# Kernel optimization log

Hardware: AMD Instinct MI355X
Metric: run time of the kernel (lower is better)

## Reference

```python
import jax, jax.numpy as jnp
import numpy as np

NUM_IN_CAPS = 1152   # 32 * 6 * 6
NUM_OUT_CAPS = 10
IN_DIM = 8
OUT_DIM = 16
ROUTING_ITERS = 3
EPS = 1e-8


def squash(s, axis=-1):
    # squash(s) = ||s||^2/(1+||s||^2) * s/||s||
    sq = jnp.sum(s * s, axis=axis, keepdims=True)
    norm = jnp.sqrt(sq + EPS)
    return (sq / (1.0 + sq)) * (s / norm)


def setup_inputs() -> dict:
    key = jax.random.key(0)
    ks = jax.random.split(key, 6)
    B = 512
    inp = jax.random.uniform(ks[0], (B, 1, 28, 28), dtype=jnp.float32)
    # conv params (He-ish scale)
    conv1_w = jax.random.normal(ks[1], (256, 1, 9, 9), dtype=jnp.float32) * 0.05
    conv1_b = jnp.zeros((256,), dtype=jnp.float32)
    conv2_w = jax.random.normal(ks[2], (256, 256, 9, 9), dtype=jnp.float32) * 0.01
    conv2_b = jnp.zeros((256,), dtype=jnp.float32)
    # capsule transform weights: [in_caps, out_caps, in_dim, out_dim]
    cap_W = jax.random.normal(ks[3], (NUM_IN_CAPS, NUM_OUT_CAPS, IN_DIM, OUT_DIM), dtype=jnp.float32) * 0.05
    return {"input": inp, "conv1_w": conv1_w, "conv1_b": conv1_b,
            "conv2_w": conv2_w, "conv2_b": conv2_b, "cap_W": cap_W}


def _conv(x, w, b, stride):
    y = jax.lax.conv_general_dilated(
        x, w, window_strides=(stride, stride), padding='VALID',
        dimension_numbers=('NCHW', 'OIHW', 'NCHW'))
    return y + b[None, :, None, None]


def capsnet_forward(input, conv1_w, conv1_b, conv2_w, conv2_b, cap_W):
    B = input.shape[0]
    h = jax.nn.relu(_conv(input, conv1_w, conv1_b, 1))   # [B,256,20,20]
    h = _conv(h, conv2_w, conv2_b, 2)                    # [B,256,6,6]
    # torch.transpose(output, 1, -1): [B,C,H,W] -> [B,W,H,C], then view(B,1152,8)
    u = jnp.transpose(h, (0, 3, 2, 1)).reshape(B, NUM_IN_CAPS, IN_DIM)
    # predicted output vectors u_hat: [B, i, j, q]
    u_hat = jnp.einsum('bip,ijpq->bijq', u, cap_W)
    # dynamic routing
    b_ij = jnp.zeros((B, NUM_IN_CAPS, NUM_OUT_CAPS), dtype=u_hat.dtype)
    v = None
    for _ in range(ROUTING_ITERS):
        c = jax.nn.softmax(b_ij, axis=2)                 # coupling over output caps
        s = jnp.einsum('bij,bijq->bjq', c, u_hat)        # [B, j, q]
        v = squash(s)                                    # [B, j, q]
        b_ij = b_ij + jnp.einsum('bijq,bjq->bij', u_hat, v)
    return v  # [B, 10, 16]


def reference(input, conv1_w, conv1_b, conv2_w, conv2_b, cap_W):
    return capsnet_forward(input, conv1_w, conv1_b, conv2_w, conv2_b, cap_W)
```

## Files before the change

### kernel.cpp

```cpp
#include <hip/hip_runtime.h>
#include <hip/hip_bf16.h>

typedef __attribute__((ext_vector_type(8))) short bf16x8;
typedef __attribute__((ext_vector_type(4))) float f32x4;

static __device__ __forceinline__ unsigned short f2bf(float x) {
    __hip_bfloat16 h = __float2bfloat16(x);
    return *(unsigned short*)&h;
}
static __device__ __forceinline__ float bflo(unsigned int w) { return __uint_as_float(w << 16); }
static __device__ __forceinline__ float bfhi(unsigned int w) { return __uint_as_float(w & 0xffff0000u); }
static __device__ __forceinline__ float bf1(unsigned short u) { return __uint_as_float(((unsigned int)u) << 16); }

typedef __attribute__((address_space(1))) const void gvoid;
typedef __attribute__((address_space(3))) void lvoid;
static __device__ __forceinline__ void gl_lds16(const void* g, void* l) {
    __builtin_amdgcn_global_load_lds((gvoid*)g, (lvoid*)l, 16, 0, 0);
}

#define PART_FLOATS 4718592

__global__ __launch_bounds__(320) void conv1_k(const float* __restrict__ in,
                                               const float* __restrict__ w,
                                               const float* __restrict__ bias,
                                               unsigned short* __restrict__ h1n) {
    int blk = blockIdx.x;
    int b = blk >> 4;
    int c0 = (blk & 15) * 16;
    __shared__ float img[784];
    __shared__ float wl[16 * 81];
    __shared__ float bl[16];
    __shared__ unsigned short tr[20 * 328];
    int tid = threadIdx.x;
    for (int t = tid; t < 784; t += 320) img[t] = in[b * 784 + t];
    for (int t = tid; t < 1296; t += 320) wl[t] = w[c0 * 81 + t];
    if (tid < 16) bl[tid] = bias[c0 + tid];
    __syncthreads();

    int co = tid / 20, oy = tid % 20;
    float wr[81];
#pragma unroll
    for (int k = 0; k < 81; k++) wr[k] = wl[co * 81 + k];
    float acc[20];
    float bv = bl[co];
#pragma unroll
    for (int ox = 0; ox < 20; ox++) acc[ox] = bv;

#pragma unroll
    for (int ky = 0; ky < 9; ky++) {
        const float* rp = &img[(oy + ky) * 28];
        float r[28];
#pragma unroll
        for (int v = 0; v < 7; v++) {
            float4 t4 = ((const float4*)rp)[v];
            r[v * 4 + 0] = t4.x; r[v * 4 + 1] = t4.y;
            r[v * 4 + 2] = t4.z; r[v * 4 + 3] = t4.w;
        }
#pragma unroll
        for (int kx = 0; kx < 9; kx++) {
            float wv = wr[ky * 9 + kx];
#pragma unroll
            for (int ox = 0; ox < 20; ox++) acc[ox] += r[ox + kx] * wv;
        }
    }
#pragma unroll
    for (int ox = 0; ox < 20; ox++)
        tr[oy * 328 + ox * 16 + co] = f2bf(fmaxf(acc[ox], 0.f));
    __syncthreads();
    for (int g = tid; g < 800; g += 320) {
        int p = g >> 1, half = g & 1;
        uint4 v = *(uint4*)&tr[(p / 20) * 328 + (p % 20) * 16 + half * 8];
        *(uint4*)&h1n[(b * 400 + p) * 256 + c0 + half * 8] = v;
    }
}

__global__ __launch_bounds__(256) void wt2_k(const float* __restrict__ w2,
                                             unsigned short* __restrict__ Wt2) {
    int cout = blockIdx.x;
    int ci = threadIdx.x;
    const float* src = w2 + (cout * 256 + ci) * 81;
#pragma unroll 1
    for (int kk = 0; kk < 81; kk++)
        Wt2[kk * 65536 + cout * 256 + ci] = f2bf(src[kk]);
#pragma unroll
    for (int kk = 81; kk < 84; kk++)
        Wt2[kk * 65536 + cout * 256 + ci] = 0;
}

__global__ __launch_bounds__(256) void wcap_k(const float* __restrict__ W,
                                              unsigned short* __restrict__ Wb) {
    int idx4 = blockIdx.x * 256 + threadIdx.x;
    float4 v = *(const float4*)&W[(size_t)idx4 * 4];
    unsigned int lo = (unsigned int)f2bf(v.x) | ((unsigned int)f2bf(v.y) << 16);
    unsigned int hi = (unsigned int)f2bf(v.z) | ((unsigned int)f2bf(v.w) << 16);
    uint2 pk; pk.x = lo; pk.y = hi;
    *(uint2*)&Wb[(size_t)idx4 * 4] = pk;
}

__global__ __launch_bounds__(256) void conv2_k(const unsigned short* __restrict__ h1n,
                                               const unsigned short* __restrict__ Wt2,
                                               const float* __restrict__ bias,
                                               float* __restrict__ u,
                                               float* __restrict__ part1,
                                               float* __restrict__ part23) {
    __shared__ unsigned short sA[2][128 * 64];
    __shared__ unsigned short sB[2][128 * 64];
    int tid = threadIdx.x;
    int m0 = blockIdx.x * 128;
    int n0 = blockIdx.y * 128;
    int slice = blockIdx.z;
    int ks = slice * 21;

    int wv = tid >> 6, lane = tid & 63;
    int wm = wv >> 1, wn = wv & 1;
    int lr = lane & 15, quad = lane >> 4;

    int lrow = lane >> 3, lslot = lane & 7;
    int kcoff = (lslot ^ lrow) * 8;
    int aG[4], bG[4];
#pragma unroll
    for (int t = 0; t < 4; t++) {
        int r = wv * 32 + t * 8 + lrow;
        int R = m0 + r;
        int b = R / 36, m = R % 36;
        int oy = m / 6, ox = m % 6;
        aG[t] = b * 102400 + oy * 10240 + ox * 512 + kcoff;
        bG[t] = (n0 + r) * 256 + kcoff;
    }

    f32x4 acc[4][4];
#pragma unroll
    for (int i = 0; i < 4; i++)
#pragma unroll
        for (int j = 0; j < 4; j++) acc[i][j] = (f32x4){0.f, 0.f, 0.f, 0.f};

    auto stage = [&](int buf, int rr) {
        int kk = ks + (rr >> 2), cr = rr & 3;
        int ky = kk / 9, kx = kk % 9;
        int aoff = ky * 5120 + kx * 256 + cr * 64;
        int boff = kk * 65536 + cr * 64;
        unsigned short* dA = &sA[buf][wv * 2048];
        unsigned short* dB = &sB[buf][wv * 2048];
#pragma unroll
        for (int t = 0; t < 4; t++)
            gl_lds16(h1n + aG[t] + aoff, dA + t * 512);
#pragma unroll
        for (int t = 0; t < 4; t++)
            gl_lds16(Wt2 + bG[t] + boff, dB + t * 512);
    };

    stage(0, 0);
    __syncthreads();

    int cur = 0;
#pragma unroll 1
    for (int rr = 0; rr < 84; rr++) {
        if (rr < 83) stage(cur ^ 1, rr + 1);
        const unsigned short* pA = &sA[cur][0];
        const unsigned short* pB = &sB[cur][0];
#pragma unroll
        for (int s = 0; s < 2; s++) {
            bf16x8 af[4], bf[4];
#pragma unroll
            for (int i = 0; i < 4; i++) {
                int arow = wm * 64 + i * 16 + lr;
                af[i] = *(bf16x8*)&pA[arow * 64 + 8 * ((s * 4 + quad) ^ (lr & 7))];
            }
#pragma unroll
            for (int j = 0; j < 4; j++) {
                int brow = wn * 64 + j * 16 + lr;
                bf[j] = *(bf16x8*)&pB[brow * 64 + 8 * ((s * 4 + quad) ^ (lr & 7))];
            }
#pragma unroll
            for (int i = 0; i < 4; i++)
#pragma unroll
                for (int j = 0; j < 4; j++)
                    acc[i][j] = __builtin_amdgcn_mfma_f32_16x16x32_bf16(
                        af[i], bf[j], acc[i][j], 0, 0, 0);
        }
        __syncthreads();
        cur ^= 1;
    }

    float* dst = (slice == 0) ? u : ((slice == 1) ? part1 : part23 + (size_t)(slice - 2) * PART_FLOATS);
#pragma unroll
    for (int j = 0; j < 4; j++) {
        int col = n0 + wn * 64 + j * 16 + lr;
        float bv = (slice == 0) ? bias[col] : 0.f;
#pragma unroll
        for (int i = 0; i < 4; i++) {
#pragma unroll
            for (int rg = 0; rg < 4; rg++) {
                int RR = m0 + wm * 64 + i * 16 + quad * 4 + rg;
                int bb = RR / 36, mm = RR % 36;
                int oyy = mm / 6, oxx = mm % 6;
                dst[bb * 9216 + oxx * 1536 + oyy * 256 + col] = acc[i][j][rg] + bv;
            }
        }
    }
}

__global__ __launch_bounds__(256) void uhat_k(const float* __restrict__ u,
                                              const float* __restrict__ p1,
                                              const float* __restrict__ p23,
                                              const unsigned short* __restrict__ Wb,
                                              unsigned short* __restrict__ uhat) {
    int i0 = blockIdx.x * 64;
    int b0 = blockIdx.y * 8;
    __shared__ float ul[8 * 576];
    __shared__ unsigned short wl[64 * 130];
    int tid = threadIdx.x;

    for (int t = tid; t < 1024; t += 256) {
        int bb = t >> 7, rq = t & 127;
        int r = rq * 4;
        size_t gidx = (size_t)(b0 + bb) * 9216 + i0 * 8 + r;
        float4 a = *(const float4*)&u[gidx];
        float4 x = *(const float4*)&p1[gidx];
        float4 y = *(const float4*)&p23[gidx];
        float4 z = *(const float4*)&p23[PART_FLOATS + gidx];
        float* d = &ul[bb * 576 + (r >> 3) * 9 + (r & 7)];
        d[0] = a.x + x.x + y.x + z.x;
        d[1] = a.y + x.y + y.y + z.y;
        d[2] = a.z + x.z + y.z + z.z;
        d[3] = a.w + x.w + y.w + z.w;
    }

    int il = tid & 63, g = tid >> 6;
    for (int j = 0; j < 10; j++) {
        __syncthreads();
        for (int t = tid; t < 4096; t += 256) {
            int li = t >> 6, cp = t & 63;
            *(unsigned int*)&wl[li * 130 + cp * 2] =
                *(const unsigned int*)&Wb[(size_t)(i0 + li) * 1280 + j * 128 + cp * 2];
        }
        __syncthreads();
#pragma unroll 1
        for (int bb = 0; bb < 8; bb++) {
            float ur[8];
#pragma unroll
            for (int p = 0; p < 8; p++) ur[p] = ul[bb * 576 + il * 9 + p];
            float a[4];
#pragma unroll
            for (int k = 0; k < 4; k++) {
                int q = g * 4 + k;
                float s = 0.f;
#pragma unroll
                for (int p = 0; p < 8; p++) s += ur[p] * bf1(wl[il * 130 + p * 16 + q]);
                a[k] = s;
            }
            unsigned int lo = (unsigned int)f2bf(a[0]) | ((unsigned int)f2bf(a[1]) << 16);
            unsigned int hi = (unsigned int)f2bf(a[2]) | ((unsigned int)f2bf(a[3]) << 16);
            uint2 pk; pk.x = lo; pk.y = hi;
            *(uint2*)&uhat[((size_t)(b0 + bb) * 10 + j) * 18432 + (size_t)(i0 + il) * 16 + g * 4] = pk;
        }
    }
}

__global__ __launch_bounds__(256) void route_k(const unsigned short* __restrict__ uhat,
                                               float* __restrict__ out) {
    int b = blockIdx.x;
    int tid = threadIdx.x;
    int w = tid >> 6, lane = tid & 63;
    int ig = lane >> 2, qh = lane & 3;
    __shared__ float b_sh[1152 * 10];
    __shared__ float s_red[4 * 160];
    __shared__ float v_sh[160];
    __shared__ float sc_sh[10];
    const unsigned short* ub = uhat + (size_t)b * 184320;

    float v_ln[10][4];

    auto finish = [&](float sp[10][4]) {
#pragma unroll
        for (int j = 0; j < 10; j++)
#pragma unroll
            for (int k = 0; k < 4; k++) {
                float t = sp[j][k];
                t += __shfl_xor(t, 4);
                t += __shfl_xor(t, 8);
                t += __shfl_xor(t, 16);
                t += __shfl_xor(t, 32);
                sp[j][k] = t;
            }
        if (ig == 0) {
#pragma unroll
            for (int j = 0; j < 10; j++) {
                f32x4 v4 = {sp[j][0], sp[j][1], sp[j][2], sp[j][3]};
                *(f32x4*)&s_red[w * 160 + j * 16 + qh * 4] = v4;
            }
        }
        __syncthreads();
        if (tid < 160) {
            float s = s_red[tid] + s_red[160 + tid] + s_red[320 + tid] + s_red[480 + tid];
            s_red[tid] = s;
        }
        __syncthreads();
        if (tid < 10) {
            float sq = 0.f;
#pragma unroll
            for (int q = 0; q < 16; q++) { float x = s_red[tid * 16 + q]; sq += x * x; }
            float norm = sqrtf(sq + 1e-8f);
            sc_sh[tid] = (sq / (1.0f + sq)) / norm;
        }
        __syncthreads();
        if (tid < 160) v_sh[tid] = s_red[tid] * sc_sh[tid >> 4];
        __syncthreads();
#pragma unroll
        for (int j = 0; j < 10; j++) {
            f32x4 v4 = *(const f32x4*)&v_sh[j * 16 + qh * 4];
            v_ln[j][0] = v4[0]; v_ln[j][1] = v4[1]; v_ln[j][2] = v4[2]; v_ln[j][3] = v4[3];
        }
        __syncthreads();
    };

    {
        float sp[10][4];
#pragma unroll
        for (int j = 0; j < 10; j++)
#pragma unroll
            for (int k = 0; k < 4; k++) sp[j][k] = 0.f;
#pragma unroll 2
        for (int r = 0; r < 18; r++) {
            int i = r * 64 + w * 16 + ig;
            const unsigned short* up = ub + (size_t)i * 16 + qh * 4;
            uint2 uh[10];
#pragma unroll
            for (int j = 0; j < 10; j++) uh[j] = *(const uint2*)(up + (size_t)j * 18432);
#pragma unroll
            for (int j = 0; j < 10; j++) {
                sp[j][0] += 0.1f * bflo(uh[j].x);
                sp[j][1] += 0.1f * bfhi(uh[j].x);
                sp[j][2] += 0.1f * bflo(uh[j].y);
                sp[j][3] += 0.1f * bfhi(uh[j].y);
            }
        }
        finish(sp);
    }

#pragma unroll 1
    for (int pass = 0; pass < 2; pass++) {
        bool first = (pass == 0);
        float sp[10][4];
#pragma unroll
        for (int j = 0; j < 10; j++)
#pragma unroll
            for (int k = 0; k < 4; k++) sp[j][k] = 0.f;
#pragma unroll 2
        for (int r = 0; r < 18; r++) {
            int i = r * 64 + w * 16 + ig;
            const unsigned short* up = ub + (size_t)i * 16 + qh * 4;
            uint2 uh[10];
#pragma unroll
            for (int j = 0; j < 10; j++) uh[j] = *(const uint2*)(up + (size_t)j * 18432);
            float d[10];
#pragma unroll
            for (int j = 0; j < 10; j++) {
                d[j] = bflo(uh[j].x) * v_ln[j][0] + bfhi(uh[j].x) * v_ln[j][1]
                     + bflo(uh[j].y) * v_ln[j][2] + bfhi(uh[j].y) * v_ln[j][3];
            }
#pragma unroll
            for (int j = 0; j < 10; j++) {
                d[j] += __shfl_xor(d[j], 1);
                d[j] += __shfl_xor(d[j], 2);
            }
            float bn[10];
            if (first) {
#pragma unroll
                for (int j = 0; j < 10; j++) bn[j] = d[j];
#pragma unroll
                for (int j = 0; j < 10; j++)
                    if (qh == (j & 3)) b_sh[i * 10 + j] = bn[j];
            } else {
#pragma unroll
                for (int j = 0; j < 10; j++) bn[j] = b_sh[i * 10 + j] + d[j];
            }
            float m = bn[0];
#pragma unroll
            for (int j = 1; j < 10; j++) m = fmaxf(m, bn[j]);
            float e[10], sum = 0.f;
#pragma unroll
            for (int j = 0; j < 10; j++) { e[j] = __expf(bn[j] - m); sum += e[j]; }
            float inv = 1.f / sum;
#pragma unroll
            for (int j = 0; j < 10; j++) {
                float c = e[j] * inv;
                sp[j][0] += c * bflo(uh[j].x);
                sp[j][1] += c * bfhi(uh[j].x);
                sp[j][2] += c * bflo(uh[j].y);
                sp[j][3] += c * bfhi(uh[j].y);
            }
        }
        finish(sp);
    }

    if (tid < 160) out[b * 160 + tid] = v_sh[tid];
}

extern "C" void kernel_launch(void* const* d_in, const int* in_sizes, int n_in,
                              void* d_out, int out_size, void* d_ws, size_t ws_size,
                              hipStream_t stream) {
    const float* input = (const float*)d_in[0];
    const float* c1w = (const float*)d_in[1];
    const float* c1b = (const float*)d_in[2];
    const float* c2w = (const float*)d_in[3];
    const float* c2b = (const float*)d_in[4];
    const float* capW = (const float*)d_in[5];
    float* out = (float*)d_out;

    const size_t U_OFF = 0;
    const size_t P1_OFF = 18874368;
    const size_t WB_OFF = 37748736;
    const size_t B_OFF = 43122688;
    const size_t WT2_BYTES = (size_t)84 * 65536 * 2;
    const size_t H1N_BYTES = 104857600;
    const size_t PART_BYTES = (size_t)PART_FLOATS * 4;
    const size_t CONV_BYTES = WT2_BYTES + H1N_BYTES + 2 * PART_BYTES;
    if (ws_size < B_OFF + CONV_BYTES) return;

    char* wsb = (char*)d_ws;
    float* u_buf = (float*)(wsb + U_OFF);
    float* part1 = (float*)(wsb + P1_OFF);
    unsigned short* Wb = (unsigned short*)(wsb + WB_OFF);
    unsigned short* Wt2 = (unsigned short*)(wsb + B_OFF);
    unsigned short* h1n = (unsigned short*)(wsb + B_OFF + WT2_BYTES);
    float* part23 = (float*)(wsb + B_OFF + WT2_BYTES + H1N_BYTES);
    unsigned short* uhatb = (unsigned short*)(wsb + B_OFF);

    wcap_k<<<1440, 256, 0, stream>>>(capW, Wb);
    wt2_k<<<256, 256, 0, stream>>>(c2w, Wt2);
    conv1_k<<<512 * 16, 320, 0, stream>>>(input, c1w, c1b, h1n);
    conv2_k<<<dim3(144, 2, 4), 256, 0, stream>>>(h1n, Wt2, c2b, u_buf, part1, part23);

    const int Cr = 256;
    for (int b0 = 0; b0 < 512; b0 += Cr) {
        uhat_k<<<dim3(18, Cr / 8), 256, 0, stream>>>(
            u_buf + (size_t)b0 * 9216, part1 + (size_t)b0 * 9216,
            part23 + (size_t)b0 * 9216, Wb, uhatb);
        route_k<<<Cr, 256, 0, stream>>>(uhatb, out + (size_t)b0 * 160);
    }
}
```

Measured before the change: 707.6 us.

## Restructure conv2 GEMM to 128x256 tiles with triple-buffered LDS pipeline

Each conv2 block now covers all 256 output channels using 512 threads, so the A-tile (im2col rows) is loaded once rather than twice across N-blocks. The double-buffered stage is replaced by a three-stage LDS ring with explicit vmcnt waits and raw barriers. The B loads are split so that half are issued between the two MFMA halves, and s_setprio is raised around the MFMA bursts. This is meant to cut redundant global/LDS traffic and hide load latency. The cost is larger LDS use (144KB) and fewer blocks (576), which may reduce occupancy.

```diff
diff --git a/kernel.cpp b/kernel.cpp
--- a/kernel.cpp
+++ b/kernel.cpp
@@ -97,36 +97,39 @@
     *(uint2*)&Wb[(size_t)idx4 * 4] = pk;
 }
 
-__global__ __launch_bounds__(256) void conv2_k(const unsigned short* __restrict__ h1n,
+__global__ __launch_bounds__(512) void conv2_k(const unsigned short* __restrict__ h1n,
                                                const unsigned short* __restrict__ Wt2,
                                                const float* __restrict__ bias,
                                                float* __restrict__ u,
                                                float* __restrict__ part1,
                                                float* __restrict__ part23) {
-    __shared__ unsigned short sA[2][128 * 64];
-    __shared__ unsigned short sB[2][128 * 64];
+    __shared__ unsigned short sA[3][128 * 64];
+    __shared__ unsigned short sB[3][256 * 64];
     int tid = threadIdx.x;
     int m0 = blockIdx.x * 128;
-    int n0 = blockIdx.y * 128;
-    int slice = blockIdx.z;
+    int slice = blockIdx.y;
     int ks = slice * 21;
 
     int wv = tid >> 6, lane = tid & 63;
-    int wm = wv >> 1, wn = wv & 1;
+    int wm = wv >> 2;
+    int wn = wv & 3;
     int lr = lane & 15, quad = lane >> 4;
-
-    int lrow = lane >> 3, lslot = lane & 7;
-    int kcoff = (lslot ^ lrow) * 8;
-    int aG[4], bG[4];
-#pragma unroll
-    for (int t = 0; t < 4; t++) {
-        int r = wv * 32 + t * 8 + lrow;
-        int R = m0 + r;
+    int rsl = lr & 7;
+
+    int srow = tid >> 3;
+    int gch = (tid & 7) ^ (srow & 7);
+    int aG[2];
+#pragma unroll
+    for (int t = 0; t < 2; t++) {
+        int R = m0 + t * 64 + srow;
         int b = R / 36, m = R % 36;
         int oy = m / 6, ox = m % 6;
-        aG[t] = b * 102400 + oy * 10240 + ox * 512 + kcoff;
-        bG[t] = (n0 + r) * 256 + kcoff;
-    }
+        aG[t] = b * 102400 + oy * 10240 + ox * 512 + gch * 8;
+    }
+    int bG[4];
+#pragma unroll
+    for (int t = 0; t < 4; t++) bG[t] = (t * 64 + srow) * 256 + gch * 8;
+    int ldst = srow * 64 + (tid & 7) * 8;
 
     f32x4 acc[4][4];
 #pragma unroll
@@ -134,67 +137,104 @@
 #pragma unroll
         for (int j = 0; j < 4; j++) acc[i][j] = (f32x4){0.f, 0.f, 0.f, 0.f};
 
-    auto stage = [&](int buf, int rr) {
-        int kk = ks + (rr >> 2), cr = rr & 3;
-        int ky = kk / 9, kx = kk % 9;
-        int aoff = ky * 5120 + kx * 256 + cr * 64;
+    auto stage0 = [&](int buf, int kt) {
+        int kk = ks + (kt >> 2), cr = kt & 3;
+        int aoff = (kk / 9) * 5120 + (kk % 9) * 256 + cr * 64;
         int boff = kk * 65536 + cr * 64;
-        unsigned short* dA = &sA[buf][wv * 2048];
-        unsigned short* dB = &sB[buf][wv * 2048];
-#pragma unroll
-        for (int t = 0; t < 4; t++)
-            gl_lds16(h1n + aG[t] + aoff, dA + t * 512);
-#pragma unroll
-        for (int t = 0; t < 4; t++)
-            gl_lds16(Wt2 + bG[t] + boff, dB + t * 512);
+        gl_lds16(h1n + aG[0] + aoff, &sA[buf][ldst]);
+        gl_lds16(h1n + aG[1] + aoff, &sA[buf][4096 + ldst]);
+        gl_lds16(Wt2 + boff + bG[0], &sB[buf][ldst]);
     };
-
-    stage(0, 0);
-    __syncthreads();
-
-    int cur = 0;
+    auto stage1 = [&](int buf, int kt) {
+        int kk = ks + (kt >> 2), cr = kt & 3;
+        int boff = kk * 65536 + cr * 64;
+        gl_lds16(Wt2 + boff + bG[1], &sB[buf][4096 + ldst]);
+        gl_lds16(Wt2 + boff + bG[2], &sB[buf][8192 + ldst]);
+        gl_lds16(Wt2 + boff + bG[3], &sB[buf][12288 + ldst]);
+    };
+
+    stage0(0, 0); stage1(0, 0);
+    stage0(1, 1); stage1(1, 1);
+
 #pragma unroll 1
-    for (int rr = 0; rr < 84; rr++) {
-        if (rr < 83) stage(cur ^ 1, rr + 1);
-        const unsigned short* pA = &sA[cur][0];
-        const unsigned short* pB = &sB[cur][0];
-#pragma unroll
-        for (int s = 0; s < 2; s++) {
-            bf16x8 af[4], bf[4];
-#pragma unroll
-            for (int i = 0; i < 4; i++) {
-                int arow = wm * 64 + i * 16 + lr;
-                af[i] = *(bf16x8*)&pA[arow * 64 + 8 * ((s * 4 + quad) ^ (lr & 7))];
-            }
-#pragma unroll
-            for (int j = 0; j < 4; j++) {
-                int brow = wn * 64 + j * 16 + lr;
-                bf[j] = *(bf16x8*)&pB[brow * 64 + 8 * ((s * 4 + quad) ^ (lr & 7))];
-            }
-#pragma unroll
-            for (int i = 0; i < 4; i++)
-#pragma unroll
-                for (int j = 0; j < 4; j++)
-                    acc[i][j] = __builtin_amdgcn_mfma_f32_16x16x32_bf16(
-                        af[i], bf[j], acc[i][j], 0, 0, 0);
-        }
-        __syncthreads();
-        cur ^= 1;
+    for (int kt = 0; kt < 84; kt++) {
+        int cb = kt % 3;
+        int pb = (kt + 2) % 3;
+        const unsigned short* pA = &sA[cb][0];
+        const unsigned short* pB = &sB[cb][0];
+        bool pf = kt < 82;
+        if (pf) {
+            stage0(pb, kt + 2);
+            asm volatile("s_waitcnt vmcnt(9)" ::: "memory");
+        } else if (kt == 82) {
+            asm volatile("s_waitcnt vmcnt(6)" ::: "memory");
+        } else {
+            asm volatile("s_waitcnt vmcnt(0)" ::: "memory");
+        }
+        __builtin_amdgcn_s_barrier();
+
+        bf16x8 af[4][2], rBlo[2][2];
+#pragma unroll
+        for (int mi = 0; mi < 4; mi++)
+#pragma unroll
+            for (int s = 0; s < 2; s++) {
+                int arow = (wm + mi * 2) * 16 + lr;
+                af[mi][s] = *(const bf16x8*)&pA[arow * 64 + 8 * ((s * 4 + quad) ^ rsl)];
+            }
+#pragma unroll
+        for (int ni = 0; ni < 2; ni++)
+#pragma unroll
+            for (int s = 0; s < 2; s++) {
+                int brow = (wn + ni * 4) * 16 + lr;
+                rBlo[ni][s] = *(const bf16x8*)&pB[brow * 64 + 8 * ((s * 4 + quad) ^ rsl)];
+            }
+        __builtin_amdgcn_s_setprio(1);
+#pragma unroll
+        for (int mi = 0; mi < 4; mi++)
+#pragma unroll
+            for (int ni = 0; ni < 2; ni++)
+#pragma unroll
+                for (int s = 0; s < 2; s++)
+                    acc[mi][ni] = __builtin_amdgcn_mfma_f32_16x16x32_bf16(
+                        af[mi][s], rBlo[ni][s], acc[mi][ni], 0, 0, 0);
+        __builtin_amdgcn_s_setprio(0);
+
+        if (pf) stage1(pb, kt + 2);
+
+        bf16x8 rBhi[2][2];
+#pragma unroll
+        for (int ni = 0; ni < 2; ni++)
+#pragma unroll
+            for (int s = 0; s < 2; s++) {
+                int brow = (wn + (ni + 2) * 4) * 16 + lr;
+                rBhi[ni][s] = *(const bf16x8*)&pB[brow * 64 + 8 * ((s * 4 + quad) ^ rsl)];
+            }
+        __builtin_amdgcn_s_setprio(1);
+#pragma unroll
+        for (int mi = 0; mi < 4; mi++)
+#pragma unroll
+            for (int ni = 0; ni < 2; ni++)
+#pragma unroll
+                for (int s = 0; s < 2; s++)
+                    acc[mi][ni + 2] = __builtin_amdgcn_mfma_f32_16x16x32_bf16(
+                        af[mi][s], rBhi[ni][s], acc[mi][ni + 2], 0, 0, 0);
+        __builtin_amdgcn_s_setprio(0);
+        __builtin_amdgcn_s_barrier();
     }
 
     float* dst = (slice == 0) ? u : ((slice == 1) ? part1 : part23 + (size_t)(slice - 2) * PART_FLOATS);
 #pragma unroll
-    for (int j = 0; j < 4; j++) {
-        int col = n0 + wn * 64 + j * 16 + lr;
+    for (int ni = 0; ni < 4; ni++) {
+        int col = (wn + ni * 4) * 16 + lr;
         float bv = (slice == 0) ? bias[col] : 0.f;
 #pragma unroll
-        for (int i = 0; i < 4; i++) {
+        for (int mi = 0; mi < 4; mi++) {
 #pragma unroll
             for (int rg = 0; rg < 4; rg++) {
-                int RR = m0 + wm * 64 + i * 16 + quad * 4 + rg;
+                int RR = m0 + (wm + mi * 2) * 16 + quad * 4 + rg;
                 int bb = RR / 36, mm = RR % 36;
                 int oyy = mm / 6, oxx = mm % 6;
-                dst[bb * 9216 + oxx * 1536 + oyy * 256 + col] = acc[i][j][rg] + bv;
+                dst[bb * 9216 + oxx * 1536 + oyy * 256 + col] = acc[mi][ni][rg] + bv;
             }
         }
     }
@@ -430,7 +470,7 @@
     wcap_k<<<1440, 256, 0, stream>>>(capW, Wb);
     wt2_k<<<256, 256, 0, stream>>>(c2w, Wt2);
     conv1_k<<<512 * 16, 320, 0, stream>>>(input, c1w, c1b, h1n);
-    conv2_k<<<dim3(144, 2, 4), 256, 0, stream>>>(h1n, Wt2, c2b, u_buf, part1, part23);
+    conv2_k<<<dim3(144, 4), 512, 0, stream>>>(h1n, Wt2, c2b, u_buf, part1, part23);
 
     const int Cr = 256;
     for (int b0 = 0; b0 < 512; b0 += Cr) {
```

Result: slower. 796.9 us (+12.6%).
